# Kernel optimization log

Hardware: AMD Instinct MI355X
Metric: run time of the kernel (lower is better)

Reference implementation:

```python
import jax, jax.numpy as jnp
import numpy as np

FILTERS = 512
DQK = FILTERS // 8  # 64


def setup_inputs() -> dict:
    key = jax.random.key(0)
    ks = jax.random.split(key, 7)
    B, H, W, C = 32, 32, 32, FILTERS
    x = jax.random.normal(ks[0], (B, H, W, C), dtype=jnp.float32)
    # 1x1 convs == per-pixel dense layers: weight [Cin, Cout], bias [Cout]
    def glorot(k, cin, cout):
        lim = np.sqrt(6.0 / (cin + cout)).astype(np.float32)
        return jax.random.uniform(k, (cin, cout), jnp.float32, -lim, lim)
    return {
        "x": x,
        "wq": glorot(ks[1], C, DQK), "bq": jnp.zeros((DQK,), jnp.float32),
        "wk": glorot(ks[2], C, DQK), "bk": jnp.zeros((DQK,), jnp.float32),
        "wv": glorot(ks[3], C, C),   "bv": jnp.zeros((C,), jnp.float32),
    }


def reference(x, wq, bq, wk, bk, wv, bv):
    B, H, W, C = x.shape
    N = H * W
    xf = x.reshape(B, N, C)                       # flatten spatial -> tokens
    q = xf @ wq + bq                              # [B, N, C//8]
    k = xf @ wk + bk                              # [B, N, C//8]
    v = xf @ wv + bv                              # [B, N, C]
    scale = 1.0 / jnp.sqrt(jnp.float32(C // 8))
    scores = jnp.einsum('bnd,bmd->bnm', q, k) * scale  # [B, N, N]
    probs = jax.nn.softmax(scores, axis=-1)
    attended = jnp.einsum('bnm,bmc->bnc', probs, v)    # [B, N, C]
    return attended.reshape(B, H, W, C) + x
```

## Files before the change

### kernel.cpp

```cpp
#include <hip/hip_runtime.h>
#include <stdint.h>

#define B_ 32
#define N_ 1024
#define C_ 512
#define D_ 64

typedef __attribute__((ext_vector_type(8))) __bf16 bf8;
typedef __attribute__((ext_vector_type(4))) float f32x4;

typedef const __attribute__((address_space(1))) void* gp_t;
typedef __attribute__((address_space(3))) void* lp_t;

__device__ inline void g2l16(const void* g, void* l) {
    __builtin_amdgcn_global_load_lds((gp_t)g, (lp_t)l, 16, 0, 0);
}

__device__ inline float b2f(unsigned short u) {
    return __uint_as_float(((unsigned)u) << 16);
}
__device__ inline unsigned short f2b(float f) {
    unsigned u = __float_as_uint(f);
    u += 0x7FFF + ((u >> 16) & 1);
    return (unsigned short)(u >> 16);
}

#define MFMA16(a, b, c) __builtin_amdgcn_mfma_f32_16x16x32_bf16((a), (b), (c), 0, 0, 0)

__global__ __launch_bounds__(256) void xcvt(const float* __restrict__ x,
                                            unsigned short* __restrict__ xb) {
    int i = blockIdx.x * 256 + threadIdx.x;
    float4 f = ((const float4*)x)[i];
    ushort4 o;
    o.x = f2b(f.x); o.y = f2b(f.y); o.z = f2b(f.z); o.w = f2b(f.w);
    ((ushort4*)xb)[i] = o;
}

__global__ __launch_bounds__(256) void wtrans_all(
    const float* __restrict__ wq, const float* __restrict__ wk,
    const float* __restrict__ wv, unsigned short* __restrict__ wt)
{
    int t = blockIdx.x * 256 + threadIdx.x;
    int co = t >> 9;
    int ci = t & 511;
    const float* src;
    int col, cout;
    if (co < 64)       { src = wq; col = co;       cout = 64;  }
    else if (co < 128) { src = wk; col = co - 64;  cout = 64;  }
    else               { src = wv; col = co - 128; cout = 512; }
    wt[t] = f2b(src[(size_t)ci * cout + col]);
}

__global__ __launch_bounds__(256) void qkv(
    const unsigned short* __restrict__ xb,
    const unsigned short* __restrict__ WT,
    const float* __restrict__ bq, const float* __restrict__ bk,
    const float* __restrict__ bv,
    unsigned short* __restrict__ q, unsigned short* __restrict__ k,
    unsigned short* __restrict__ vT)
{
    const int rb = blockIdx.x;
    const int cb = blockIdx.y;
    const int tid = threadIdx.x;
    const int lane = tid & 63;
    const int wave = tid >> 6;
    const int wm = wave >> 1, wn = wave & 1;
    const int lr = lane & 15;
    const int lk = lane >> 4;

    __shared__ unsigned short SM[32768];
    unsigned short* TB = SM;

    const int row0 = rb * 128;
    const int col0 = cb * 128;

    f32x4 zero4 = {0.f, 0.f, 0.f, 0.f};
    f32x4 acc[4][4];
    #pragma unroll
    for (int i = 0; i < 4; ++i)
        #pragma unroll
        for (int j = 0; j < 4; ++j) acc[i][j] = zero4;

    auto stage = [&](int buf, int kk) {
        unsigned short* As = SM + buf * 8192;
        unsigned short* Bs = SM + 16384 + buf * 8192;
        #pragma unroll
        for (int i = 0; i < 4; ++i) {
            int f = wave * 4 + i;
            int t = f >> 1, kq = f & 1;
            g2l16(xb + (size_t)(row0 + t * 16 + lr) * C_ + kk + kq * 32 + lk * 8,
                  &As[f * 512]);
            g2l16(WT + (size_t)(col0 + t * 16 + lr) * C_ + kk + kq * 32 + lk * 8,
                  &Bs[f * 512]);
        }
    };

    stage(0, 0);
    __syncthreads();
    int cur = 0;
    for (int kk = 64; kk < C_; kk += 64) {
        const unsigned short* As = SM + cur * 8192;
        const unsigned short* Bs = SM + 16384 + cur * 8192;
        bf8 a[2][4], bb[2][4];
        #pragma unroll
        for (int kq = 0; kq < 2; ++kq) {
            #pragma unroll
            for (int ti = 0; ti < 4; ++ti)
                a[kq][ti] = *(const bf8*)&As[((wm * 4 + ti) * 2 + kq) * 512 + lane * 8];
            #pragma unroll
            for (int tj = 0; tj < 4; ++tj)
                bb[kq][tj] = *(const bf8*)&Bs[((wn * 4 + tj) * 2 + kq) * 512 + lane * 8];
        }
        __builtin_amdgcn_sched_barrier(0);
        stage(cur ^ 1, kk);
        #pragma unroll
        for (int kq = 0; kq < 2; ++kq)
            #pragma unroll
            for (int ti = 0; ti < 4; ++ti)
                #pragma unroll
                for (int tj = 0; tj < 4; ++tj)
                    acc[ti][tj] = MFMA16(a[kq][ti], bb[kq][tj], acc[ti][tj]);
        __syncthreads();
        cur ^= 1;
    }
    {
        const unsigned short* As = SM + cur * 8192;
        const unsigned short* Bs = SM + 16384 + cur * 8192;
        #pragma unroll
        for (int kq = 0; kq < 2; ++kq) {
            bf8 a[4], bb[4];
            #pragma unroll
            for (int ti = 0; ti < 4; ++ti)
                a[ti] = *(const bf8*)&As[((wm * 4 + ti) * 2 + kq) * 512 + lane * 8];
            #pragma unroll
            for (int tj = 0; tj < 4; ++tj)
                bb[tj] = *(const bf8*)&Bs[((wn * 4 + tj) * 2 + kq) * 512 + lane * 8];
            #pragma unroll
            for (int ti = 0; ti < 4; ++ti)
                #pragma unroll
                for (int tj = 0; tj < 4; ++tj)
                    acc[ti][tj] = MFMA16(a[ti], bb[tj], acc[ti][tj]);
        }
    }

    if (cb == 0) {
        unsigned short* outp = (wn == 0) ? q : k;
        const float* bias = (wn == 0) ? bq : bk;
        #pragma unroll
        for (int ti = 0; ti < 4; ++ti)
            #pragma unroll
            for (int tj = 0; tj < 4; ++tj) {
                int col = tj * 16 + lr;
                float bi = bias[col];
                #pragma unroll
                for (int r = 0; r < 4; ++r) {
                    int row = row0 + wm * 64 + ti * 16 + lk * 4 + r;
                    outp[(size_t)row * D_ + col] = f2b(acc[ti][tj][r] + bi);
                }
            }
    } else {
        const int colv = (cb - 1) * 128;
        __syncthreads();
        #pragma unroll
        for (int ti = 0; ti < 4; ++ti)
            #pragma unroll
            for (int tj = 0; tj < 4; ++tj) {
                int c = wn * 64 + tj * 16 + lr;
                float bi = bv[colv + c];
                int tok = wm * 64 + ti * 16 + lk * 4;
                ushort4 o;
                o.x = f2b(acc[ti][tj][0] + bi);
                o.y = f2b(acc[ti][tj][1] + bi);
                o.z = f2b(acc[ti][tj][2] + bi);
                o.w = f2b(acc[ti][tj][3] + bi);
                *(ushort4*)&TB[c * 132 + tok] = o;
            }
        __syncthreads();
        const int b  = row0 >> 10;
        const int n0 = row0 & 1023;
        #pragma unroll
        for (int i = 0; i < 16; ++i) {
            int idx = tid + 256 * i;
            int c = idx >> 5, ch = idx & 31;
            ushort4 t4 = *(const ushort4*)&TB[c * 132 + ch * 4];
            *(ushort4*)&vT[((size_t)(b * C_ + colv + c)) * N_ + n0 + ch * 4] = t4;
        }
    }
}

#define SLD 1032
__global__ __launch_bounds__(256) void scores(
    const unsigned short* __restrict__ q,
    const unsigned short* __restrict__ k,
    unsigned short* __restrict__ P)
{
    const int qt = blockIdx.x, b = blockIdx.y;
    const int tid = threadIdx.x, lane = tid & 63, wave = tid >> 6;
    const int lr = lane & 15, lk = lane >> 4;
    __shared__ unsigned short S[16 * SLD];

    const int n0 = qt * 16;
    const unsigned short* qrow = q + (size_t)(b * N_ + n0 + lr) * D_ + lk * 8;
    bf8 qa0 = *(const bf8*)(qrow);
    bf8 qa1 = *(const bf8*)(qrow + 32);

    const int m0w = wave * 256;
    #pragma unroll 4
    for (int mt = 0; mt < 16; ++mt) {
        int m = m0w + mt * 16;
        const unsigned short* krow = k + (size_t)(b * N_ + m + lr) * D_ + lk * 8;
        bf8 kb0 = *(const bf8*)(krow);
        bf8 kb1 = *(const bf8*)(krow + 32);
        f32x4 s = {0.f, 0.f, 0.f, 0.f};
        s = MFMA16(qa0, kb0, s);
        s = MFMA16(qa1, kb1, s);
        #pragma unroll
        for (int r = 0; r < 4; ++r)
            S[(lk * 4 + r) * SLD + m + lr] = f2b(s[r] * 0.125f);
    }
    __syncthreads();

    #pragma unroll
    for (int rr4 = 0; rr4 < 4; ++rr4) {
        int rr = wave * 4 + rr4;
        float vals[16];
        float mx = -1e30f;
        #pragma unroll
        for (int j = 0; j < 16; ++j) {
            vals[j] = b2f(S[rr * SLD + j * 64 + lane]);
            mx = fmaxf(mx, vals[j]);
        }
        #pragma unroll
        for (int off = 32; off; off >>= 1) mx = fmaxf(mx, __shfl_xor(mx, off));
        float sum = 0.f;
        #pragma unroll
        for (int j = 0; j < 16; ++j) { vals[j] = __expf(vals[j] - mx); sum += vals[j]; }
        #pragma unroll
        for (int off = 32; off; off >>= 1) sum += __shfl_xor(sum, off);
        float inv = 1.f / sum;
        unsigned short* pp = P + (size_t)(b * N_ + n0 + rr) * N_;
        #pragma unroll
        for (int j = 0; j < 16; ++j) pp[j * 64 + lane] = f2b(vals[j] * inv);
    }
}

__global__ __launch_bounds__(256) void pv(
    const unsigned short* __restrict__ P,
    const unsigned short* __restrict__ vT,
    const float* __restrict__ x,
    float* __restrict__ out)
{
    const int m0 = blockIdx.x * 128, c0 = blockIdx.y * 128, b = blockIdx.z;
    const int tid = threadIdx.x, lane = tid & 63, wave = tid >> 6;
    const int wm = wave >> 1, wn = wave & 1;
    const int lr = lane & 15, lk = lane >> 4;

    __shared__ unsigned short As[2][8192];
    __shared__ unsigned short Bs[2][8192];

    f32x4 zero4 = {0.f, 0.f, 0.f, 0.f};
    f32x4 acc[4][4];
    #pragma unroll
    for (int i = 0; i < 4; ++i)
        #pragma unroll
        for (int j = 0; j < 4; ++j) acc[i][j] = zero4;

    const unsigned short* Pb = P  + (size_t)b * N_ * N_;
    const unsigned short* Vb = vT + (size_t)b * C_ * N_;

    auto stage = [&](int buf, int kk) {
        #pragma unroll
        for (int i = 0; i < 4; ++i) {
            int f = wave * 4 + i;
            int t = f >> 1, kq = f & 1;
            g2l16(Pb + (size_t)(m0 + t * 16 + lr) * N_ + kk + kq * 32 + lk * 8,
                  &As[buf][f * 512]);
            g2l16(Vb + (size_t)(c0 + t * 16 + lr) * N_ + kk + kq * 32 + lk * 8,
                  &Bs[buf][f * 512]);
        }
    };

    stage(0, 0);
    __syncthreads();
    int cur = 0;
    for (int kk = 64; kk < N_; kk += 64) {
        bf8 a[2][4], bb[2][4];
        #pragma unroll
        for (int kq = 0; kq < 2; ++kq) {
            #pragma unroll
            for (int ti = 0; ti < 4; ++ti)
                a[kq][ti] = *(const bf8*)&As[cur][((wm * 4 + ti) * 2 + kq) * 512 + lane * 8];
            #pragma unroll
            for (int tj = 0; tj < 4; ++tj)
                bb[kq][tj] = *(const bf8*)&Bs[cur][((wn * 4 + tj) * 2 + kq) * 512 + lane * 8];
        }
        __builtin_amdgcn_sched_barrier(0);
        stage(cur ^ 1, kk);
        #pragma unroll
        for (int kq = 0; kq < 2; ++kq)
            #pragma unroll
            for (int ti = 0; ti < 4; ++ti)
                #pragma unroll
                for (int tj = 0; tj < 4; ++tj)
                    acc[ti][tj] = MFMA16(a[kq][ti], bb[kq][tj], acc[ti][tj]);
        __syncthreads();
        cur ^= 1;
    }
    {
        #pragma unroll
        for (int kq = 0; kq < 2; ++kq) {
            bf8 a[4], bb[4];
            #pragma unroll
            for (int ti = 0; ti < 4; ++ti)
                a[ti] = *(const bf8*)&As[cur][((wm * 4 + ti) * 2 + kq) * 512 + lane * 8];
            #pragma unroll
            for (int tj = 0; tj < 4; ++tj)
                bb[tj] = *(const bf8*)&Bs[cur][((wn * 4 + tj) * 2 + kq) * 512 + lane * 8];
            #pragma unroll
            for (int ti = 0; ti < 4; ++ti)
                #pragma unroll
                for (int tj = 0; tj < 4; ++tj)
                    acc[ti][tj] = MFMA16(a[ti], bb[tj], acc[ti][tj]);
        }
    }

    #pragma unroll
    for (int ti = 0; ti < 4; ++ti)
        #pragma unroll
        for (int tj = 0; tj < 4; ++tj) {
            int col = c0 + wn * 64 + tj * 16 + lr;
            #pragma unroll
            for (int r = 0; r < 4; ++r) {
                int row = m0 + wm * 64 + ti * 16 + lk * 4 + r;
                size_t idx = (size_t)(b * N_ + row) * C_ + col;
                out[idx] = acc[ti][tj][r] + x[idx];
            }
        }
}

extern "C" void kernel_launch(void* const* d_in, const int* in_sizes, int n_in,
                              void* d_out, int out_size, void* d_ws, size_t ws_size,
                              hipStream_t stream) {
    (void)in_sizes; (void)n_in; (void)out_size; (void)ws_size;
    const float* xf = (const float*)d_in[0];
    const float* wq = (const float*)d_in[1];
    const float* bq = (const float*)d_in[2];
    const float* wk = (const float*)d_in[3];
    const float* bk = (const float*)d_in[4];
    const float* wv = (const float*)d_in[5];
    const float* bv = (const float*)d_in[6];
    float* out = (float*)d_out;

    char* ws = (char*)d_ws;
    unsigned short* qb  = (unsigned short*)(ws);
    unsigned short* kb  = (unsigned short*)(ws + 4194304);
    unsigned short* vTb = (unsigned short*)(ws + 8388608);
    unsigned short* WT  = (unsigned short*)(ws + 41943040);
    unsigned short* xb  = (unsigned short*)(ws + 42598400);
    unsigned short* Pb  = (unsigned short*)(ws + 41943040);

    xcvt<<<16384, 256, 0, stream>>>(xf, xb);
    wtrans_all<<<1280, 256, 0, stream>>>(wq, wk, wv, WT);
    qkv<<<dim3(256, 5), 256, 0, stream>>>(xb, WT, bq, bk, bv, qb, kb, vTb);
    scores<<<dim3(64, 32), 256, 0, stream>>>(qb, kb, Pb);
    pv<<<dim3(8, 4, 32), 256, 0, stream>>>(Pb, vTb, xf, out);
}
```

Measured before the change: 288.0 us.

## Keep two async LDS stages in flight with vmcnt-based waits in GEMM kernels

Restructures the double-buffered main loops of the QKV projection and PV GEMM kernels so that two global-to-LDS stages are issued up front. Each iteration waits only on the older stage via s_waitcnt vmcnt(8) instead of draining all loads with __syncthreads. The next stage is issued into the buffer just read, after an lgkmcnt wait and a barrier. The goal is to hide more global load latency behind MFMA work, at the cost of an extra barrier per iteration and a dependence on hand-counted vmcnt values.

```diff
diff --git a/kernel.cpp b/kernel.cpp
--- a/kernel.cpp
+++ b/kernel.cpp
@@ -26,6 +26,31 @@
 }
 
 #define MFMA16(a, b, c) __builtin_amdgcn_mfma_f32_16x16x32_bf16((a), (b), (c), 0, 0, 0)
+
+__device__ __forceinline__ void ld_frags(const unsigned short* As, const unsigned short* Bs,
+                                         int wm, int wn, int lane,
+                                         bf8 (&a)[2][4], bf8 (&bb)[2][4]) {
+    #pragma unroll
+    for (int kq = 0; kq < 2; ++kq) {
+        #pragma unroll
+        for (int ti = 0; ti < 4; ++ti)
+            a[kq][ti] = *(const bf8*)&As[((wm * 4 + ti) * 2 + kq) * 512 + lane * 8];
+        #pragma unroll
+        for (int tj = 0; tj < 4; ++tj)
+            bb[kq][tj] = *(const bf8*)&Bs[((wn * 4 + tj) * 2 + kq) * 512 + lane * 8];
+    }
+}
+
+__device__ __forceinline__ void do_mfma(const bf8 (&a)[2][4], const bf8 (&bb)[2][4],
+                                        f32x4 (&acc)[4][4]) {
+    #pragma unroll
+    for (int kq = 0; kq < 2; ++kq)
+        #pragma unroll
+        for (int ti = 0; ti < 4; ++ti)
+            #pragma unroll
+            for (int tj = 0; tj < 4; ++tj)
+                acc[ti][tj] = MFMA16(a[kq][ti], bb[kq][tj], acc[ti][tj]);
+}
 
 __global__ __launch_bounds__(256) void xcvt(const float* __restrict__ x,
                                             unsigned short* __restrict__ xb) {
@@ -96,51 +121,33 @@
     };
 
     stage(0, 0);
-    __syncthreads();
+    stage(1, 64);
     int cur = 0;
-    for (int kk = 64; kk < C_; kk += 64) {
-        const unsigned short* As = SM + cur * 8192;
-        const unsigned short* Bs = SM + 16384 + cur * 8192;
-        bf8 a[2][4], bb[2][4];
-        #pragma unroll
-        for (int kq = 0; kq < 2; ++kq) {
-            #pragma unroll
-            for (int ti = 0; ti < 4; ++ti)
-                a[kq][ti] = *(const bf8*)&As[((wm * 4 + ti) * 2 + kq) * 512 + lane * 8];
-            #pragma unroll
-            for (int tj = 0; tj < 4; ++tj)
-                bb[kq][tj] = *(const bf8*)&Bs[((wn * 4 + tj) * 2 + kq) * 512 + lane * 8];
-        }
-        __builtin_amdgcn_sched_barrier(0);
-        stage(cur ^ 1, kk);
-        #pragma unroll
-        for (int kq = 0; kq < 2; ++kq)
-            #pragma unroll
-            for (int ti = 0; ti < 4; ++ti)
-                #pragma unroll
-                for (int tj = 0; tj < 4; ++tj)
-                    acc[ti][tj] = MFMA16(a[kq][ti], bb[kq][tj], acc[ti][tj]);
-        __syncthreads();
+    for (int t = 0; t < 6; ++t) {
+        asm volatile("s_waitcnt vmcnt(8)" ::: "memory");
+        __builtin_amdgcn_s_barrier();
+        bf8 a[2][4], bb[2][4];
+        ld_frags(SM + cur * 8192, SM + 16384 + cur * 8192, wm, wn, lane, a, bb);
+        asm volatile("s_waitcnt lgkmcnt(0)" ::: "memory");
+        __builtin_amdgcn_s_barrier();
+        stage(cur, (t + 2) * 64);
+        do_mfma(a, bb, acc);
         cur ^= 1;
     }
     {
-        const unsigned short* As = SM + cur * 8192;
-        const unsigned short* Bs = SM + 16384 + cur * 8192;
-        #pragma unroll
-        for (int kq = 0; kq < 2; ++kq) {
-            bf8 a[4], bb[4];
-            #pragma unroll
-            for (int ti = 0; ti < 4; ++ti)
-                a[ti] = *(const bf8*)&As[((wm * 4 + ti) * 2 + kq) * 512 + lane * 8];
-            #pragma unroll
-            for (int tj = 0; tj < 4; ++tj)
-                bb[tj] = *(const bf8*)&Bs[((wn * 4 + tj) * 2 + kq) * 512 + lane * 8];
-            #pragma unroll
-            for (int ti = 0; ti < 4; ++ti)
-                #pragma unroll
-                for (int tj = 0; tj < 4; ++tj)
-                    acc[ti][tj] = MFMA16(a[ti], bb[tj], acc[ti][tj]);
-        }
+        asm volatile("s_waitcnt vmcnt(8)" ::: "memory");
+        __builtin_amdgcn_s_barrier();
+        bf8 a[2][4], bb[2][4];
+        ld_frags(SM + cur * 8192, SM + 16384 + cur * 8192, wm, wn, lane, a, bb);
+        do_mfma(a, bb, acc);
+        cur ^= 1;
+    }
+    {
+        asm volatile("s_waitcnt vmcnt(0)" ::: "memory");
+        __builtin_amdgcn_s_barrier();
+        bf8 a[2][4], bb[2][4];
+        ld_frags(SM + cur * 8192, SM + 16384 + cur * 8192, wm, wn, lane, a, bb);
+        do_mfma(a, bb, acc);
     }
 
     if (cb == 0) {
@@ -281,47 +288,33 @@
     };
 
     stage(0, 0);
-    __syncthreads();
+    stage(1, 64);
     int cur = 0;
-    for (int kk = 64; kk < N_; kk += 64) {
-        bf8 a[2][4], bb[2][4];
-        #pragma unroll
-        for (int kq = 0; kq < 2; ++kq) {
-            #pragma unroll
-            for (int ti = 0; ti < 4; ++ti)
-                a[kq][ti] = *(const bf8*)&As[cur][((wm * 4 + ti) * 2 + kq) * 512 + lane * 8];
-            #pragma unroll
-            for (int tj = 0; tj < 4; ++tj)
-                bb[kq][tj] = *(const bf8*)&Bs[cur][((wn * 4 + tj) * 2 + kq) * 512 + lane * 8];
-        }
-        __builtin_amdgcn_sched_barrier(0);
-        stage(cur ^ 1, kk);
-        #pragma unroll
-        for (int kq = 0; kq < 2; ++kq)
-            #pragma unroll
-            for (int ti = 0; ti < 4; ++ti)
-                #pragma unroll
-                for (int tj = 0; tj < 4; ++tj)
-                    acc[ti][tj] = MFMA16(a[kq][ti], bb[kq][tj], acc[ti][tj]);
-        __syncthreads();
+    for (int t = 0; t < 14; ++t) {
+        asm volatile("s_waitcnt vmcnt(8)" ::: "memory");
+        __builtin_amdgcn_s_barrier();
+        bf8 a[2][4], bb[2][4];
+        ld_frags(&As[cur][0], &Bs[cur][0], wm, wn, lane, a, bb);
+        asm volatile("s_waitcnt lgkmcnt(0)" ::: "memory");
+        __builtin_amdgcn_s_barrier();
+        stage(cur, (t + 2) * 64);
+        do_mfma(a, bb, acc);
         cur ^= 1;
     }
     {
-        #pragma unroll
-        for (int kq = 0; kq < 2; ++kq) {
-            bf8 a[4], bb[4];
-            #pragma unroll
-            for (int ti = 0; ti < 4; ++ti)
-                a[ti] = *(const bf8*)&As[cur][((wm * 4 + ti) * 2 + kq) * 512 + lane * 8];
-            #pragma unroll
-            for (int tj = 0; tj < 4; ++tj)
-                bb[tj] = *(const bf8*)&Bs[cur][((wn * 4 + tj) * 2 + kq) * 512 + lane * 8];
-            #pragma unroll
-            for (int ti = 0; ti < 4; ++ti)
-                #pragma unroll
-                for (int tj = 0; tj < 4; ++tj)
-                    acc[ti][tj] = MFMA16(a[ti], bb[tj], acc[ti][tj]);
-        }
+        asm volatile("s_waitcnt vmcnt(8)" ::: "memory");
+        __builtin_amdgcn_s_barrier();
+        bf8 a[2][4], bb[2][4];
+        ld_frags(&As[cur][0], &Bs[cur][0], wm, wn, lane, a, bb);
+        do_mfma(a, bb, acc);
+        cur ^= 1;
+    }
+    {
+        asm volatile("s_waitcnt vmcnt(0)" ::: "memory");
+        __builtin_amdgcn_s_barrier();
+        bf8 a[2][4], bb[2][4];
+        ld_frags(&As[cur][0], &Bs[cur][0], wm, wn, lane, a, bb);
+        do_mfma(a, bb, acc);
     }
 
     #pragma unroll
```

Measured after the change: 284.4 us. Within noise of the previous version (-1.2%).
